# Optimization experiments

Hardware: AMD Instinct MI355X
Metric: run time of the kernel (lower is better)

Reference implementation:

```python
import jax, jax.numpy as jnp
import numpy as np

NBINS = 128
LOGSCALE = False


def setup_inputs() -> dict:
    key = jax.random.key(0)
    X = jax.random.normal(key, (2048, 32768), dtype=jnp.float32)
    return {"X": X}


def reference(X) -> jnp.ndarray:
    # Flatten all non-leading dims (mirrors X.view(len(X), -1))
    X = X.reshape(X.shape[0], -1)
    ns = X.shape[1]
    nfreqs = 2 * (NBINS - 1) + 1          # window length (255)
    hop = nfreqs // 2
    starts = jnp.arange(0, ns - nfreqs + 1, hop)          # [nwin]
    idx = starts[:, None] + jnp.arange(nfreqs)[None, :]    # [nwin, nfreqs]
    W = X[:, idx]                          # [ntrials, nwin, nfreqs] gathered windows
    # One batched rfft + fused |.|^2 and mean over windows (Welch average)
    S = jnp.mean(jnp.abs(jnp.fft.rfft(W, axis=-1)) ** 2, axis=1)  # [ntrials, NBINS]
    if LOGSCALE:
        S = jnp.log10(S)
    return S
```

## Files before the change

kernel.cpp:

```cpp
#include <hip/hip_runtime.h>
#include <hip/hip_bf16.h>

#define NS     32768
#define NROWS  2048
#define HOP    127
#define NW     257
#define NB     128
#define WTILE  16
#define NT     17
#define TWOPI_255 0.02463994236f

typedef _Float16 f16;
typedef __attribute__((ext_vector_type(2))) _Float16 f16x2;
typedef __attribute__((ext_vector_type(4))) _Float16 f16x4;
typedef __attribute__((ext_vector_type(8))) _Float16 f16x8;
typedef __attribute__((ext_vector_type(4))) float f32x4;

__device__ inline f32x4 load4u(const char* p) {
    f32x4 v;
    __builtin_memcpy(&v, p, 16);
    return v;
}

__global__ __launch_bounds__(256)
void basis_kernel(f16* __restrict__ bt) {
    const int t  = blockIdx.x * 256 + threadIdx.x;
    const int fi = t >> 6;
    const int l  = t & 63;
    const int cq = fi >> 3;
    const int nt = (fi >> 2) & 1;
    const int kk = fi & 3;
    const int is_sin = cq >> 2;
    const int f  = (cq & 3) * 32 + nt * 16 + (l & 15);
    int m = (f * (kk * 32 + (l >> 4) * 8)) % 255;
    f16x8 v;
    #pragma unroll
    for (int j = 0; j < 8; ++j) {
        const float ang = (float)m * TWOPI_255;
        v[j] = (f16)(is_sin ? __sinf(ang) : __cosf(ang));
        m += f; if (m >= 255) m -= 255;
    }
    *(f16x8*)(bt + (size_t)t * 8) = v;
}

__global__ __launch_bounds__(512, 6)
void psd_kernel(const float* __restrict__ X, const f16* __restrict__ bt,
                float* __restrict__ out) {
    const int row  = blockIdx.x;
    const int tid  = threadIdx.x;
    const int lane = tid & 63;
    const int cq   = tid >> 6;
    const int r16  = lane & 15;
    const int kg   = lane >> 4;
    const int is_sin = cq >> 2;

    __shared__ alignas(16) f16 atile[4][WTILE * 256];
    __shared__ float scol[256];

    const char* __restrict__ xrow = (const char*)(X + (size_t)row * NS);

    const int sw  = tid >> 5;
    const int sq  = tid & 31;

    const uint voff_f = (uint)((sw * HOP + sq * 4) * 4);
    const uint voff_r = (uint)((sw * HOP + 252 - sq * 4) * 4);
    const uint vclamp = (uint)((NS - 4) * 4);

    f32x4 fv = load4u(xrow + voff_f);
    f32x4 rv = load4u(xrow + voff_r);

    f16x8 bfrag[2][4];
    {
        const char* bp = (const char*)bt + (uint)(cq * 8192 + lane * 16);
        #pragma unroll
        for (int nt = 0; nt < 2; ++nt)
            #pragma unroll
            for (int kk = 0; kk < 4; ++kk)
                bfrag[nt][kk] = *(const f16x8*)(bp + (uint)((nt * 4 + kk) * 1024));
    }

    char* const lds = (char*)&atile[0][0];

    const uint swz  = (uint)((sw & 7) << 4);
    const uint wr_p = ((uint)(sw * 512 + sq * 8)) ^ swz;
    const uint wr_m = ((uint)(sw * 512 + sq * 8 + 256)) ^ swz;
    const uint rswz = (uint)((r16 & 7) << 4);
    uint rd[4];
    #pragma unroll
    for (int kk = 0; kk < 4; ++kk)
        rd[kk] = ((uint)(r16 * 512 + is_sin * 256 + kg * 16 + kk * 64)) ^ rswz;

    auto fold_write = [&](char* wp, bool valid) {
        const f16x2 fp01 = __builtin_bit_cast(f16x2, __builtin_amdgcn_cvt_pkrtz(fv[0], fv[1]));
        const f16x2 fp23 = __builtin_bit_cast(f16x2, __builtin_amdgcn_cvt_pkrtz(fv[2], fv[3]));
        const f16x2 rp01 = __builtin_bit_cast(f16x2, __builtin_amdgcn_cvt_pkrtz(rv[3], rv[2]));
        const f16x2 rp23 = __builtin_bit_cast(f16x2, __builtin_amdgcn_cvt_pkrtz(rv[1], rv[0]));
        const f16x2 yp01 = fp01 + rp01, yp23 = fp23 + rp23;
        const f16x2 ym01 = fp01 - rp01, ym23 = fp23 - rp23;
        f16x4 h0, h1;
        h0[0] = yp01[0]; h0[1] = yp01[1]; h0[2] = yp23[0]; h0[3] = yp23[1];
        h1[0] = ym01[0]; h1[1] = ym01[1]; h1[2] = ym23[0]; h1[3] = ym23[1];
        if (sq == 0) { h0[0] = (f16)fv[0]; h1[0] = (f16)0.0f; }
        if (!valid) {
            #pragma unroll
            for (int j = 0; j < 4; ++j) { h0[j] = (f16)0.0f; h1[j] = (f16)0.0f; }
        }
        *(f16x4*)(wp + wr_p) = h0;
        *(f16x4*)(wp + wr_m) = h1;
    };

    fold_write(lds + (0 << 13), true);
    {
        const uint tb = (uint)(1 * WTILE * HOP * 4);
        fv = load4u(xrow + (voff_f + tb));
        rv = load4u(xrow + (voff_r + tb));
    }
    fold_write(lds + (1 << 13), true);
    {
        const uint tb = (uint)(2 * WTILE * HOP * 4);
        fv = load4u(xrow + (voff_f + tb));
        rv = load4u(xrow + (voff_r + tb));
    }
    asm volatile("s_waitcnt lgkmcnt(0)" ::: "memory");
    __builtin_amdgcn_s_barrier();
    asm volatile("" ::: "memory");

    float ssum0 = 0.f, ssum1 = 0.f;

    for (int mt = 0; mt < NT; ++mt) {
        const char* ap = lds + ((mt & 3) << 13);

        f32x4 acc0 = {0,0,0,0}, acc1 = {0,0,0,0};
        __builtin_amdgcn_s_setprio(1);
        #pragma unroll
        for (int kk = 0; kk < 4; ++kk) {
            const f16x8 af = *(const f16x8*)(ap + rd[kk]);
            acc0 = __builtin_amdgcn_mfma_f32_16x16x32_f16(af, bfrag[0][kk], acc0, 0, 0, 0);
            acc1 = __builtin_amdgcn_mfma_f32_16x16x32_f16(af, bfrag[1][kk], acc1, 0, 0, 0);
        }
        __builtin_amdgcn_s_setprio(0);
        #pragma unroll
        for (int r = 0; r < 4; ++r) {
            ssum0 += acc0[r] * acc0[r];
            ssum1 += acc1[r] * acc1[r];
        }

        if (mt + 2 < NT) {
            char* wp = lds + (((mt + 2) & 3) << 13);
            const bool valid = (mt + 2 != 16) || (sw == 0);
            fold_write(wp, valid);
            if (mt + 3 < NT) {
                const uint tb = (uint)((mt + 3) * WTILE * HOP * 4);
                fv = load4u(xrow + min(voff_f + tb, vclamp));
                rv = load4u(xrow + min(voff_r + tb, vclamp));
            }
        }
        if (mt & 1) {
            asm volatile("s_waitcnt lgkmcnt(0)" ::: "memory");
            __builtin_amdgcn_s_barrier();
            asm volatile("" ::: "memory");
        }
    }

    {
        float v = ssum0;
        v += __shfl_xor(v, 16, 64);
        v += __shfl_xor(v, 32, 64);
        if (kg == 0) scol[is_sin * 128 + (cq & 3) * 32 + r16] = v;
        float w = ssum1;
        w += __shfl_xor(w, 16, 64);
        w += __shfl_xor(w, 32, 64);
        if (kg == 0) scol[is_sin * 128 + (cq & 3) * 32 + 16 + r16] = w;
    }
    __syncthreads();
    if (tid < NB) {
        out[(size_t)row * NB + tid] = (scol[tid] + scol[tid + NB]) * (1.0f / 257.0f);
    }
}

extern "C" void kernel_launch(void* const* d_in, const int* in_sizes, int n_in,
                              void* d_out, int out_size, void* d_ws, size_t ws_size,
                              hipStream_t stream) {
    const float* X = (const float*)d_in[0];
    float* out = (float*)d_out;
    f16* bt = (f16*)d_ws;
    (void)in_sizes; (void)n_in; (void)ws_size; (void)out_size;
    basis_kernel<<<dim3(16), dim3(256), 0, stream>>>(bt);
    psd_kernel<<<dim3(NROWS), dim3(512), 0, stream>>>(X, bt, out);
}
```

Baseline: 53.52 us.

## Split window tiles across wave groups, widen per-wave frequency tile to four

Each wave now holds four basis fragments (64 frequency columns) instead of two and handles only every other window tile, alternating by wave group. Each A-fragment LDS read now feeds four MFMAs instead of two, halving per-tile LDS read traffic. Partial power sums from the two wave groups are combined through a doubled shared-memory scratch. The cost is more basis registers per wave, so the launch-bounds occupancy hint drops from 6 to 4 blocks, which may reduce latency hiding.

```diff
diff --git a/kernel.cpp b/kernel.cpp
--- a/kernel.cpp
+++ b/kernel.cpp
@@ -43,7 +43,7 @@
     *(f16x8*)(bt + (size_t)t * 8) = v;
 }
 
-__global__ __launch_bounds__(512, 6)
+__global__ __launch_bounds__(512, 4)
 void psd_kernel(const float* __restrict__ X, const f16* __restrict__ bt,
                 float* __restrict__ out) {
     const int row  = blockIdx.x;
@@ -52,10 +52,12 @@
     const int cq   = tid >> 6;
     const int r16  = lane & 15;
     const int kg   = lane >> 4;
-    const int is_sin = cq >> 2;
+    const int mg   = cq >> 2;
+    const int hs   = (cq >> 1) & 1;
+    const int ng   = cq & 1;
 
     __shared__ alignas(16) f16 atile[4][WTILE * 256];
-    __shared__ float scol[256];
+    __shared__ float scol[2][256];
 
     const char* __restrict__ xrow = (const char*)(X + (size_t)row * NS);
 
@@ -69,14 +71,16 @@
     f32x4 fv = load4u(xrow + voff_f);
     f32x4 rv = load4u(xrow + voff_r);
 
-    f16x8 bfrag[2][4];
+    f16x8 bfrag[4][4];
     {
-        const char* bp = (const char*)bt + (uint)(cq * 8192 + lane * 16);
+        const char* bp = (const char*)bt + (uint)(lane * 16);
         #pragma unroll
-        for (int nt = 0; nt < 2; ++nt)
+        for (int m = 0; m < 4; ++m) {
+            const int fi0 = hs * 32 + (ng * 2 + (m >> 1)) * 8 + (m & 1) * 4;
             #pragma unroll
             for (int kk = 0; kk < 4; ++kk)
-                bfrag[nt][kk] = *(const f16x8*)(bp + (uint)((nt * 4 + kk) * 1024));
+                bfrag[m][kk] = *(const f16x8*)(bp + (uint)((fi0 + kk) * 1024));
+        }
     }
 
     char* const lds = (char*)&atile[0][0];
@@ -88,7 +92,7 @@
     uint rd[4];
     #pragma unroll
     for (int kk = 0; kk < 4; ++kk)
-        rd[kk] = ((uint)(r16 * 512 + is_sin * 256 + kg * 16 + kk * 64)) ^ rswz;
+        rd[kk] = ((uint)(r16 * 512 + hs * 256 + kg * 16 + kk * 64)) ^ rswz;
 
     auto fold_write = [&](char* wp, bool valid) {
         const f16x2 fp01 = __builtin_bit_cast(f16x2, __builtin_amdgcn_cvt_pkrtz(fv[0], fv[1]));
@@ -125,24 +129,29 @@
     __builtin_amdgcn_s_barrier();
     asm volatile("" ::: "memory");
 
-    float ssum0 = 0.f, ssum1 = 0.f;
+    float ssum[4] = {0.f, 0.f, 0.f, 0.f};
 
     for (int mt = 0; mt < NT; ++mt) {
-        const char* ap = lds + ((mt & 3) << 13);
-
-        f32x4 acc0 = {0,0,0,0}, acc1 = {0,0,0,0};
-        __builtin_amdgcn_s_setprio(1);
-        #pragma unroll
-        for (int kk = 0; kk < 4; ++kk) {
-            const f16x8 af = *(const f16x8*)(ap + rd[kk]);
-            acc0 = __builtin_amdgcn_mfma_f32_16x16x32_f16(af, bfrag[0][kk], acc0, 0, 0, 0);
-            acc1 = __builtin_amdgcn_mfma_f32_16x16x32_f16(af, bfrag[1][kk], acc1, 0, 0, 0);
-        }
-        __builtin_amdgcn_s_setprio(0);
-        #pragma unroll
-        for (int r = 0; r < 4; ++r) {
-            ssum0 += acc0[r] * acc0[r];
-            ssum1 += acc1[r] * acc1[r];
+        if ((mt & 1) == mg) {
+            const char* ap = lds + ((mt & 3) << 13);
+            f32x4 acc0 = {0,0,0,0}, acc1 = {0,0,0,0}, acc2 = {0,0,0,0}, acc3 = {0,0,0,0};
+            __builtin_amdgcn_s_setprio(1);
+            #pragma unroll
+            for (int kk = 0; kk < 4; ++kk) {
+                const f16x8 af = *(const f16x8*)(ap + rd[kk]);
+                acc0 = __builtin_amdgcn_mfma_f32_16x16x32_f16(af, bfrag[0][kk], acc0, 0, 0, 0);
+                acc1 = __builtin_amdgcn_mfma_f32_16x16x32_f16(af, bfrag[1][kk], acc1, 0, 0, 0);
+                acc2 = __builtin_amdgcn_mfma_f32_16x16x32_f16(af, bfrag[2][kk], acc2, 0, 0, 0);
+                acc3 = __builtin_amdgcn_mfma_f32_16x16x32_f16(af, bfrag[3][kk], acc3, 0, 0, 0);
+            }
+            __builtin_amdgcn_s_setprio(0);
+            #pragma unroll
+            for (int r = 0; r < 4; ++r) {
+                ssum[0] += acc0[r] * acc0[r];
+                ssum[1] += acc1[r] * acc1[r];
+                ssum[2] += acc2[r] * acc2[r];
+                ssum[3] += acc3[r] * acc3[r];
+            }
         }
 
         if (mt + 2 < NT) {
@@ -162,19 +171,18 @@
         }
     }
 
-    {
-        float v = ssum0;
+    #pragma unroll
+    for (int m = 0; m < 4; ++m) {
+        float v = ssum[m];
         v += __shfl_xor(v, 16, 64);
         v += __shfl_xor(v, 32, 64);
-        if (kg == 0) scol[is_sin * 128 + (cq & 3) * 32 + r16] = v;
-        float w = ssum1;
-        w += __shfl_xor(w, 16, 64);
-        w += __shfl_xor(w, 32, 64);
-        if (kg == 0) scol[is_sin * 128 + (cq & 3) * 32 + 16 + r16] = w;
+        if (kg == 0) scol[mg][hs * 128 + ng * 64 + m * 16 + r16] = v;
     }
     __syncthreads();
     if (tid < NB) {
-        out[(size_t)row * NB + tid] = (scol[tid] + scol[tid + NB]) * (1.0f / 257.0f);
+        const float s = scol[0][tid] + scol[0][tid + NB]
+                      + scol[1][tid] + scol[1][tid + NB];
+        out[(size_t)row * NB + tid] = s * (1.0f / 257.0f);
     }
 }
 
```

After: 63.35 us. +18.4%, slower.
